# Kernel tuning notes

Measured on AMD Instinct MI355X. Metric: run time of the kernel, lower is better.

## Reference

```python
import jax, jax.numpy as jnp
import numpy as np

N_HEADS = 16
D_MODEL = 2048
D_HEAD = D_MODEL // N_HEADS
B, T = 4, 2048


def setup_inputs() -> dict:
    key = jax.random.key(0)
    k1, k2, k3 = jax.random.split(key, 3)
    x = jax.random.normal(k1, (B, T, D_MODEL), dtype=jnp.float32)
    # stored as [in, out] so y = x @ W + b (equivalent to torch Linear with W_torch = W.T)
    W_qkv = jax.random.normal(k2, (D_MODEL, 3 * D_MODEL), dtype=jnp.float32) * (D_MODEL ** -0.5)
    b_qkv = jnp.zeros((3 * D_MODEL,), dtype=jnp.float32)
    W_out = jax.random.normal(k3, (D_MODEL, D_MODEL), dtype=jnp.float32) * (D_MODEL ** -0.5)
    b_out = jnp.zeros((D_MODEL,), dtype=jnp.float32)
    return {"x": x, "W_qkv": W_qkv, "b_qkv": b_qkv, "W_out": W_out, "b_out": b_out}


def reference(x, W_qkv, b_qkv, W_out, b_out):
    b, t, c = x.shape
    qkv = x @ W_qkv + b_qkv                       # [B,T,3C]
    q, k, v = jnp.split(qkv, 3, axis=-1)
    # [B,T,C] -> [B,H,T,Dh]
    def heads(u):
        return u.reshape(b, t, N_HEADS, D_HEAD).transpose(0, 2, 1, 3)
    q, k, v = heads(q), heads(k), heads(v)
    scale = 1.0 / D_HEAD                          # muP scale: 1/d_head (not 1/sqrt)
    att = jnp.einsum('bhqd,bhkd->bhqk', q, k) * scale
    causal = jnp.tril(jnp.ones((t, t), dtype=bool))
    att = jnp.where(causal, att, -jnp.inf)
    att = jax.nn.softmax(att, axis=-1)
    y = jnp.einsum('bhqk,bhkd->bhqd', att, v)     # [B,H,T,Dh]
    y = y.transpose(0, 2, 1, 3).reshape(b, t, c)
    return y @ W_out + b_out
```

## Files before the change

### kernel.cpp

```cpp
#include <hip/hip_runtime.h>
#include <hip/hip_bf16.h>
#include <cstdint>


using f32x4  = __attribute__((ext_vector_type(4))) float;
using u32x4  = __attribute__((ext_vector_type(4))) unsigned int;
using u16x8  = __attribute__((ext_vector_type(8))) unsigned short;
using u16x4  = __attribute__((ext_vector_type(4))) unsigned short;
using bf16x8 = __attribute__((ext_vector_type(8))) __bf16;

__device__ __forceinline__ unsigned short f2bf(float f) {
  unsigned int u = __builtin_bit_cast(unsigned int, f);
  u += 0x7fffu + ((u >> 16) & 1u);
  return (unsigned short)(u >> 16);
}

__device__ __forceinline__ void async_copy16(const unsigned short* g, unsigned short* l) {
  __builtin_amdgcn_global_load_lds(
      (const __attribute__((address_space(1))) unsigned int*)g,
      (__attribute__((address_space(3))) unsigned int*)l,
      16, 0, 0);
}

__global__ __launch_bounds__(256) void cast_x_kernel(const float* __restrict__ x,
                                                     unsigned short* __restrict__ xb) {
  const size_t i = (size_t)blockIdx.x * 256 + threadIdx.x;
  const float* p = x + i * 8;
  f32x4 a = *(const f32x4*)p;
  f32x4 b = *(const f32x4*)(p + 4);
  u16x8 o;
#pragma unroll
  for (int e = 0; e < 4; ++e) { o[e] = f2bf(a[e]); o[e + 4] = f2bf(b[e]); }
  *(u32x4*)(xb + i * 8) = __builtin_bit_cast(u32x4, o);
}

__global__ __launch_bounds__(256) void transpose_cast_w(const float* __restrict__ W,
                                                        unsigned short* __restrict__ WT,
                                                        int K, int N) {
  __shared__ unsigned short tbuf[64 * 68];
  const int tid = threadIdx.x;
  const int k0 = blockIdx.x * 64, n0 = blockIdx.y * 64;
#pragma unroll
  for (int it = 0; it < 4; ++it) {
    int c = it * 256 + tid;
    int kl = c >> 4, n4 = (c & 15) * 4;
    f32x4 v = *(const f32x4*)(W + (size_t)(k0 + kl) * N + n0 + n4);
#pragma unroll
    for (int e = 0; e < 4; ++e) tbuf[(n4 + e) * 68 + kl] = f2bf(v[e]);
  }
  __syncthreads();
#pragma unroll
  for (int it = 0; it < 2; ++it) {
    int c = it * 256 + tid;
    int nl = c >> 3, k8 = (c & 7) * 8;
    u16x4 lo = *(const u16x4*)&tbuf[nl * 68 + k8];
    u16x4 hi = *(const u16x4*)&tbuf[nl * 68 + k8 + 4];
    u16x8 o;
#pragma unroll
    for (int e = 0; e < 4; ++e) { o[e] = lo[e]; o[e + 4] = hi[e]; }
    *(u32x4*)(WT + (size_t)(n0 + nl) * K + k0 + k8) = __builtin_bit_cast(u32x4, o);
  }
}

__global__ __launch_bounds__(256) void transpose_v_kernel(const unsigned short* __restrict__ qkv,
                                                          unsigned short* __restrict__ vT) {
  __shared__ unsigned short tbuf[64 * 68];
  const int tid = threadIdx.x;
  const int t0 = blockIdx.x * 64;
  const int d0 = blockIdx.y * 64;
  const int bh = blockIdx.z;
  const int b = bh >> 4, h = bh & 15;
#pragma unroll
  for (int it = 0; it < 2; ++it) {
    int c = it * 256 + tid;
    int tl = c >> 3, d8 = (c & 7) * 8;
    u32x4 v = *(const u32x4*)(qkv + (size_t)(b * 2048 + t0 + tl) * 6144 + 4096 + h * 128 + d0 + d8);
    u16x8 u = __builtin_bit_cast(u16x8, v);
#pragma unroll
    for (int e = 0; e < 8; ++e) tbuf[(d8 + e) * 68 + tl] = u[e];
  }
  __syncthreads();
#pragma unroll
  for (int it = 0; it < 2; ++it) {
    int c = it * 256 + tid;
    int dl = c >> 3, t8 = (c & 7) * 8;
    u16x4 lo = *(const u16x4*)&tbuf[dl * 68 + t8];
    u16x4 hi = *(const u16x4*)&tbuf[dl * 68 + t8 + 4];
    u16x8 o;
#pragma unroll
    for (int e = 0; e < 4; ++e) { o[e] = lo[e]; o[e + 4] = hi[e]; }
    *(u32x4*)(vT + ((size_t)bh * 128 + d0 + dl) * 2048 + t0 + t8) = __builtin_bit_cast(u32x4, o);
  }
}


__device__ __forceinline__ void stage_region(const unsigned short* gsrc, int K,
                                             unsigned short* region, int tid) {
#pragma unroll
  for (int l = 0; l < 2; ++l) {
    const int s = l * 512 + tid;
    const int row = s >> 3, c = s & 7;
    const int g = c ^ (row & 7);
    async_copy16(gsrc + (size_t)row * K + g * 8, region + s * 8);
  }
}

__device__ __forceinline__ bf16x8 lds_frag(const unsigned short* region, int row, int ch) {
  return __builtin_bit_cast(bf16x8,
      *(const u32x4*)(region + row * 64 + ((ch ^ (row & 7)) * 8)));
}

template <bool OUT_BF16>
__global__ __launch_bounds__(512, 1) void gemm_bt(const unsigned short* __restrict__ A,
                                                  const unsigned short* __restrict__ BT,
                                                  const float* __restrict__ bias,
                                                  void* __restrict__ Cout,
                                                  int M, int N, int K) {
  __shared__ unsigned short As[32768];
  __shared__ unsigned short Bs[32768];

  const int tid  = threadIdx.x;
  const int lane = tid & 63;
  const int wave = tid >> 6;
  const int r16  = lane & 15;
  const int quad = lane >> 4;
  const int wm   = (wave >> 2) * 128;
  const int wn   = (wave & 3) * 64;
  const int rhA  = wave >> 2;
  const int rhB  = (wave >> 1) & 1;
  const int brow = wn & 64;

  const int orig = blockIdx.y * gridDim.x + blockIdx.x;
  const int xcd  = orig & 7;
  const int kb   = orig >> 3;
  const int MC   = gridDim.x >> 3;
  const int m0   = (xcd * MC + (kb % MC)) * 256;
  const int n0   = (kb / MC) * 256;

  const unsigned short* Ag = A + (size_t)m0 * K;
  const unsigned short* Bg = BT + (size_t)n0 * K;
  const int NT = K >> 6;

  f32x4 acc[8][4] = {};

#pragma unroll
  for (int tt = 0; tt < 2; ++tt) {
    const size_t kk0 = (size_t)tt * 64;
    unsigned short* Ad = As + tt * 16384;
    unsigned short* Bd = Bs + tt * 16384;
    stage_region(Bg + kk0, K, Bd, tid);
    stage_region(Bg + (size_t)128 * K + kk0, K, Bd + 8192, tid);
    stage_region(Ag + kk0, K, Ad, tid);
    stage_region(Ag + (size_t)128 * K + kk0, K, Ad + 8192, tid);
  }
  asm volatile("s_waitcnt vmcnt(8)" ::: "memory");
  __builtin_amdgcn_s_barrier();

  for (int t = 0; t < NT; ++t) {
    const int buf = t & 1;
    const unsigned short* Ar = As + buf * 16384 + rhA * 8192;
    const unsigned short* Br = Bs + buf * 16384 + rhB * 8192;
    unsigned short* Asg = As + buf * 16384;
    unsigned short* Bsg = Bs + buf * 16384;
    const bool pre = (t + 2 < NT);
    const size_t kpre = (size_t)(t + 2) << 6;

    bf16x8 a0[4][2], a1[4][2], b0[2][2], b1[2][2];

#pragma unroll
    for (int mi = 0; mi < 4; ++mi)
#pragma unroll
      for (int kk = 0; kk < 2; ++kk)
        a0[mi][kk] = lds_frag(Ar, mi * 16 + r16, kk * 4 + quad);
#pragma unroll
    for (int nj = 0; nj < 2; ++nj)
#pragma unroll
      for (int kk = 0; kk < 2; ++kk)
        b0[nj][kk] = lds_frag(Br, brow + nj * 16 + r16, kk * 4 + quad);
    __builtin_amdgcn_s_barrier();
    asm volatile("s_waitcnt lgkmcnt(0)" ::: "memory");
    __builtin_amdgcn_sched_barrier(0);
    __builtin_amdgcn_s_setprio(1);
#pragma unroll
    for (int mi = 0; mi < 4; ++mi)
#pragma unroll
      for (int nj = 0; nj < 2; ++nj)
#pragma unroll
        for (int kk = 0; kk < 2; ++kk)
          acc[mi][nj] = __builtin_amdgcn_mfma_f32_16x16x32_bf16(a0[mi][kk], b0[nj][kk], acc[mi][nj], 0, 0, 0);
    __builtin_amdgcn_s_setprio(0);
    __builtin_amdgcn_s_barrier();

#pragma unroll
    for (int nj = 0; nj < 2; ++nj)
#pragma unroll
      for (int kk = 0; kk < 2; ++kk)
        b1[nj][kk] = lds_frag(Br, brow + 32 + nj * 16 + r16, kk * 4 + quad);
    __builtin_amdgcn_s_barrier();
    asm volatile("s_waitcnt lgkmcnt(0)" ::: "memory");
    __builtin_amdgcn_sched_barrier(0);
    __builtin_amdgcn_s_setprio(1);
#pragma unroll
    for (int mi = 0; mi < 4; ++mi)
#pragma unroll
      for (int nj = 0; nj < 2; ++nj)
#pragma unroll
        for (int kk = 0; kk < 2; ++kk)
          acc[mi][nj + 2] = __builtin_amdgcn_mfma_f32_16x16x32_bf16(a0[mi][kk], b1[nj][kk], acc[mi][nj + 2], 0, 0, 0);
    __builtin_amdgcn_s_setprio(0);
    __builtin_amdgcn_s_barrier();

#pragma unroll
    for (int mi = 0; mi < 4; ++mi)
#pragma unroll
      for (int kk = 0; kk < 2; ++kk)
        a1[mi][kk] = lds_frag(Ar, 64 + mi * 16 + r16, kk * 4 + quad);
    if (pre) {
      stage_region(Bg + kpre, K, Bsg, tid);
      stage_region(Bg + (size_t)128 * K + kpre, K, Bsg + 8192, tid);
    }
    __builtin_amdgcn_s_barrier();
    asm volatile("s_waitcnt lgkmcnt(0)" ::: "memory");
    __builtin_amdgcn_sched_barrier(0);
    __builtin_amdgcn_s_setprio(1);
#pragma unroll
    for (int mi = 0; mi < 4; ++mi)
#pragma unroll
      for (int nj = 0; nj < 2; ++nj)
#pragma unroll
        for (int kk = 0; kk < 2; ++kk)
          acc[mi + 4][nj + 2] = __builtin_amdgcn_mfma_f32_16x16x32_bf16(a1[mi][kk], b1[nj][kk], acc[mi + 4][nj + 2], 0, 0, 0);
    __builtin_amdgcn_s_setprio(0);
    __builtin_amdgcn_s_barrier();

    if (pre) {
      stage_region(Ag + kpre, K, Asg, tid);
      stage_region(Ag + (size_t)128 * K + kpre, K, Asg + 8192, tid);
    }
    __builtin_amdgcn_s_barrier();
    __builtin_amdgcn_sched_barrier(0);
    __builtin_amdgcn_s_setprio(1);
#pragma unroll
    for (int mi = 0; mi < 4; ++mi)
#pragma unroll
      for (int nj = 0; nj < 2; ++nj)
#pragma unroll
        for (int kk = 0; kk < 2; ++kk)
          acc[mi + 4][nj] = __builtin_amdgcn_mfma_f32_16x16x32_bf16(a1[mi][kk], b0[nj][kk], acc[mi + 4][nj], 0, 0, 0);
    __builtin_amdgcn_s_setprio(0);
    if (pre) { asm volatile("s_waitcnt vmcnt(8)" ::: "memory"); }
    else     { asm volatile("s_waitcnt vmcnt(0)" ::: "memory"); }
    __builtin_amdgcn_s_barrier();
  }

#pragma unroll
  for (int nj = 0; nj < 4; ++nj) {
    const int n = n0 + wn + nj * 16 + r16;
    const float bv = bias[n];
#pragma unroll
    for (int mi = 0; mi < 8; ++mi) {
      const int mr = m0 + wm + mi * 16 + quad * 4;
#pragma unroll
      for (int r = 0; r < 4; ++r) {
        float v = acc[mi][nj][r] + bv;
        if constexpr (OUT_BF16)
          ((unsigned short*)Cout)[(size_t)(mr + r) * N + n] = f2bf(v);
        else
          ((float*)Cout)[(size_t)(mr + r) * N + n] = v;
      }
    }
  }
}

__global__ __launch_bounds__(256) void attn_kernel(const unsigned short* __restrict__ qkv,
                                                   const unsigned short* __restrict__ vT,
                                                   unsigned short* __restrict__ y) {
  __shared__ unsigned short Ks[64 * 128];
  __shared__ unsigned short Vs[128 * 64];
  __shared__ unsigned short Ps[4][32 * 72];

  const int tid  = threadIdx.x;
  const int lane = tid & 63;
  const int wave = tid >> 6;
  const int r16  = lane & 15;
  const int quad = lane >> 4;
  const int qt   = 15 - blockIdx.x;
  const int q0   = qt * 128;
  const int bh   = blockIdx.y;
  const int b    = bh >> 4, h = bh & 15;
  const int wq0  = q0 + wave * 32;
  unsigned short* pl = Ps[wave];

  bf16x8 aq[2][4];
#pragma unroll
  for (int mi = 0; mi < 2; ++mi) {
    const unsigned short* qp = qkv + (size_t)(b * 2048 + wq0 + mi * 16 + r16) * 6144 + h * 128;
#pragma unroll
    for (int kc = 0; kc < 4; ++kc)
      aq[mi][kc] = __builtin_bit_cast(bf16x8, *(const u32x4*)(qp + kc * 32 + quad * 8));
  }

  f32x4 o[2][8] = {};
  float rs_l[2][4] = {};

  const unsigned short* kbase = qkv + (size_t)b * 2048 * 6144 + 2048 + h * 128;
  const unsigned short* vbase = vT + (size_t)bh * 128 * 2048;
  const int ntiles = 2 * qt + 2;

  for (int t = 0; t < ntiles; ++t) {
    const int kv0 = t * 64;
#pragma unroll
    for (int it = 0; it < 4; ++it) {
      const int slot = it * 256 + tid;
      const int row = slot >> 4, c = slot & 15;
      const int g = c ^ (row & 15);
      async_copy16(kbase + (size_t)(kv0 + row) * 6144 + g * 8, Ks + slot * 8);
    }
#pragma unroll
    for (int it = 0; it < 4; ++it) {
      const int slot = it * 256 + tid;
      const int dr = slot >> 3, c = slot & 7;
      const int g = c ^ (dr & 7);
      async_copy16(vbase + (size_t)dr * 2048 + kv0 + g * 8, Vs + slot * 8);
    }
    __syncthreads();

    f32x4 s[2][4] = {};
#pragma unroll
    for (int kc = 0; kc < 4; ++kc) {
#pragma unroll
      for (int nt = 0; nt < 4; ++nt) {
        const int krow = nt * 16 + r16;
        const int chunk = kc * 4 + quad;
        bf16x8 bk = __builtin_bit_cast(bf16x8,
            *(const u32x4*)(Ks + (krow * 16 + (chunk ^ (krow & 15))) * 8));
#pragma unroll
        for (int mi = 0; mi < 2; ++mi)
          s[mi][nt] = __builtin_amdgcn_mfma_f32_16x16x32_bf16(aq[mi][kc], bk, s[mi][nt], 0, 0, 0);
      }
    }

    const bool need_mask = (kv0 + 64 > wq0);
#pragma unroll
    for (int mi = 0; mi < 2; ++mi) {
#pragma unroll
      for (int r = 0; r < 4; ++r) {
        const int qg = wq0 + mi * 16 + quad * 4 + r;
        float acc = 0.0f;
#pragma unroll
        for (int nt = 0; nt < 4; ++nt) {
          float e = exp2f(s[mi][nt][r] * 0.0112718764f);
          if (need_mask && (kv0 + nt * 16 + r16 > qg)) e = 0.0f;
          acc += e;
          pl[(mi * 16 + quad * 4 + r) * 72 + nt * 16 + r16] = f2bf(e);
        }
        rs_l[mi][r] += acc;
      }
    }

#pragma unroll
    for (int kc = 0; kc < 2; ++kc) {
      bf16x8 ap[2];
#pragma unroll
      for (int mi = 0; mi < 2; ++mi)
        ap[mi] = __builtin_bit_cast(bf16x8,
            *(const u32x4*)(pl + (mi * 16 + r16) * 72 + kc * 32 + quad * 8));
#pragma unroll
      for (int d = 0; d < 8; ++d) {
        const int drow = d * 16 + r16;
        const int chunk = kc * 4 + quad;
        bf16x8 bv = __builtin_bit_cast(bf16x8,
            *(const u32x4*)(Vs + (drow * 8 + (chunk ^ (drow & 7))) * 8));
#pragma unroll
        for (int mi = 0; mi < 2; ++mi)
          o[mi][d] = __builtin_amdgcn_mfma_f32_16x16x32_bf16(ap[mi], bv, o[mi][d], 0, 0, 0);
      }
    }
    __syncthreads();
  }

#pragma unroll
  for (int mi = 0; mi < 2; ++mi) {
#pragma unroll
    for (int r = 0; r < 4; ++r) {
      float rs = rs_l[mi][r];
#pragma unroll
      for (int off = 8; off >= 1; off >>= 1) rs += __shfl_xor(rs, off);
      const float inv = 1.0f / rs;
      const int qg = wq0 + mi * 16 + quad * 4 + r;
      unsigned short* yp = y + (size_t)(b * 2048 + qg) * 2048 + h * 128;
#pragma unroll
      for (int d = 0; d < 8; ++d)
        yp[d * 16 + r16] = f2bf(o[mi][d][r] * inv);
    }
  }
}

extern "C" void kernel_launch(void* const* d_in, const int* in_sizes, int n_in,
                              void* d_out, int out_size, void* d_ws, size_t ws_size,
                              hipStream_t stream) {
  const float* x     = (const float*)d_in[0];
  const float* W_qkv = (const float*)d_in[1];
  const float* b_qkv = (const float*)d_in[2];
  const float* W_out = (const float*)d_in[3];
  const float* b_out = (const float*)d_in[4];

  unsigned short* ws  = (unsigned short*)d_ws;
  unsigned short* qkv = ws;
  unsigned short* vT  = ws + 50331648;
  unsigned short* xb  = ws + 67108864;
  unsigned short* wqT = ws + 83886080;
  unsigned short* woT = ws + 96468992;
  unsigned short* y   = xb;

  cast_x_kernel<<<8192, 256, 0, stream>>>(x, xb);
  transpose_cast_w<<<dim3(32, 96), 256, 0, stream>>>(W_qkv, wqT, 2048, 6144);
  transpose_cast_w<<<dim3(32, 32), 256, 0, stream>>>(W_out, woT, 2048, 2048);
  gemm_bt<true><<<dim3(32, 24), 512, 0, stream>>>(xb, wqT, b_qkv, qkv, 8192, 6144, 2048);
  transpose_v_kernel<<<dim3(32, 2, 64), 256, 0, stream>>>(qkv, vT);
  attn_kernel<<<dim3(16, 64), 256, 0, stream>>>(qkv, vT, y);
  gemm_bt<false><<<dim3(32, 8), 512, 0, stream>>>(y, woT, b_out, d_out, 8192, 2048, 2048);
}
```

Before: 688.3 us.

## Prefetch next K/V tile into registers to overlap loads with attention compute

Replaces the per-tile async global-to-LDS copies with register prefetching. The next K/V tile is loaded into registers while the current tile is computed, then written to LDS after a barrier. It also swaps the grid order so heavy query tiles across all batch-heads are scheduled first, and adds a min-blocks-per-CU launch bound of 3. This costs extra registers and a second LDS store pass, and the occupancy hint may force spills.

Measured after the change: 768.2 us. +11.6%, slower.

```diff
diff --git a/kernel.cpp b/kernel.cpp
--- a/kernel.cpp
+++ b/kernel.cpp
@@ -272,9 +272,9 @@
   }
 }
 
-__global__ __launch_bounds__(256) void attn_kernel(const unsigned short* __restrict__ qkv,
-                                                   const unsigned short* __restrict__ vT,
-                                                   unsigned short* __restrict__ y) {
+__global__ __launch_bounds__(256, 3) void attn_kernel(const unsigned short* __restrict__ qkv,
+                                                      const unsigned short* __restrict__ vT,
+                                                      unsigned short* __restrict__ y) {
   __shared__ unsigned short Ks[64 * 128];
   __shared__ unsigned short Vs[128 * 64];
   __shared__ unsigned short Ps[4][32 * 72];
@@ -284,9 +284,9 @@
   const int wave = tid >> 6;
   const int r16  = lane & 15;
   const int quad = lane >> 4;
-  const int qt   = 15 - blockIdx.x;
+  const int qt   = 15 - blockIdx.y;
   const int q0   = qt * 128;
-  const int bh   = blockIdx.y;
+  const int bh   = blockIdx.x;
   const int b    = bh >> 4, h = bh & 15;
   const int wq0  = q0 + wave * 32;
   unsigned short* pl = Ps[wave];
@@ -307,23 +307,40 @@
   const unsigned short* vbase = vT + (size_t)bh * 128 * 2048;
   const int ntiles = 2 * qt + 2;
 
+  const int kg = (tid & 15) ^ (tid >> 4);
+  const int vg = (tid & 7) ^ ((tid >> 3) & 7);
+  const int krow0 = tid >> 4;
+  const int vrow0 = tid >> 3;
+
+  u32x4 kreg[4], vreg[4];
+
+#define ATTN_LOADREGS(KV0)                                                              \
+  {                                                                                     \
+    _Pragma("unroll")                                                                   \
+    for (int it = 0; it < 4; ++it)                                                      \
+      kreg[it] = *(const u32x4*)(kbase + (size_t)((KV0) + it * 16 + krow0) * 6144 + kg * 8); \
+    _Pragma("unroll")                                                                   \
+    for (int it = 0; it < 4; ++it)                                                      \
+      vreg[it] = *(const u32x4*)(vbase + (size_t)(it * 32 + vrow0) * 2048 + (KV0) + vg * 8); \
+  }
+
+  ATTN_LOADREGS(0);
+
   for (int t = 0; t < ntiles; ++t) {
     const int kv0 = t * 64;
-#pragma unroll
-    for (int it = 0; it < 4; ++it) {
-      const int slot = it * 256 + tid;
-      const int row = slot >> 4, c = slot & 15;
-      const int g = c ^ (row & 15);
-      async_copy16(kbase + (size_t)(kv0 + row) * 6144 + g * 8, Ks + slot * 8);
-    }
-#pragma unroll
-    for (int it = 0; it < 4; ++it) {
-      const int slot = it * 256 + tid;
-      const int dr = slot >> 3, c = slot & 7;
-      const int g = c ^ (dr & 7);
-      async_copy16(vbase + (size_t)dr * 2048 + kv0 + g * 8, Vs + slot * 8);
-    }
-    __syncthreads();
+    asm volatile("s_waitcnt vmcnt(0)" ::: "memory");
+    __builtin_amdgcn_s_barrier();
+    __builtin_amdgcn_sched_barrier(0);
+#pragma unroll
+    for (int it = 0; it < 4; ++it)
+      *(u32x4*)(Ks + (it * 256 + tid) * 8) = kreg[it];
+#pragma unroll
+    for (int it = 0; it < 4; ++it)
+      *(u32x4*)(Vs + (it * 256 + tid) * 8) = vreg[it];
+    asm volatile("s_waitcnt lgkmcnt(0)" ::: "memory");
+    if (t + 1 < ntiles) ATTN_LOADREGS(kv0 + 64);
+    __builtin_amdgcn_s_barrier();
+    __builtin_amdgcn_sched_barrier(0);
 
     f32x4 s[2][4] = {};
 #pragma unroll
@@ -376,7 +393,6 @@
           o[mi][d] = __builtin_amdgcn_mfma_f32_16x16x32_bf16(ap[mi], bv, o[mi][d], 0, 0, 0);
       }
     }
-    __syncthreads();
   }
 
 #pragma unroll
@@ -394,6 +410,7 @@
         yp[d * 16 + r16] = f2bf(o[mi][d][r] * inv);
     }
   }
+#undef ATTN_LOADREGS
 }
 
 extern "C" void kernel_launch(void* const* d_in, const int* in_sizes, int n_in,
@@ -418,6 +435,6 @@
   transpose_cast_w<<<dim3(32, 32), 256, 0, stream>>>(W_out, woT, 2048, 2048);
   gemm_bt<true><<<dim3(32, 24), 512, 0, stream>>>(xb, wqT, b_qkv, qkv, 8192, 6144, 2048);
   transpose_v_kernel<<<dim3(32, 2, 64), 256, 0, stream>>>(qkv, vT);
-  attn_kernel<<<dim3(16, 64), 256, 0, stream>>>(qkv, vT, y);
+  attn_kernel<<<dim3(64, 16), 256, 0, stream>>>(qkv, vT, y);
   gemm_bt<false><<<dim3(32, 8), 512, 0, stream>>>(y, woT, b_out, d_out, 8192, 2048, 2048);
 }
```
